# Performance work log

Measured on AMD Instinct MI355X. Metric: run time of the kernel, lower is better.

Reference implementation:

```python
import jax, jax.numpy as jnp
import numpy as np

K = 20  # kNN neighbours (conf.k)

def knn_edge_feats(x, k):
    """x: [B, C, N] -> edge features [B, 2C, N, k] (central || neighbor-central)."""
    xt = jnp.swapaxes(x, 1, 2)                       # [B, N, C]
    sq = jnp.sum(xt * xt, axis=2, keepdims=True)     # [B, N, 1]
    dist = -2.0 * jnp.einsum('bnc,bcm->bnm', xt, x) + sq + jnp.swapaxes(sq, 1, 2)  # [B,N,N]
    idx = jnp.argsort(dist, axis=2)[:, :, 1:k + 1]   # [B, N, k], skip self (col 0)
    nbrs = jax.vmap(lambda xb, ib: xb[:, ib])(x, idx)  # [B, C, N, k]
    central = x[:, :, :, None]                        # [B, C, N, 1]
    return jnp.concatenate([jnp.broadcast_to(central, nbrs.shape), nbrs - central], axis=1)

def edge_conv(x, w, b, k):
    """1x1 conv over edge features, max over k.  x:[B,C,N], w:[Fout,2C], b:[Fout]."""
    ee = knn_edge_feats(x, k)                                   # [B, 2C, N, k]
    y = jnp.einsum('oc,bcnk->bonk', w, ee) + b[None, :, None, None]
    return jnp.max(y, axis=3)                                   # [B, Fout, N]

def setup_inputs() -> dict:
    key = jax.random.key(0)
    ks = iter(jax.random.split(key, 32))
    B, N = 16, 2048
    d = {}
    d['x'] = jax.random.normal(next(ks), (B, 3, N), dtype=jnp.float32)
    def w(shape, scale):
        return jax.random.normal(next(ks), shape, dtype=jnp.float32) * scale
    d['ec0_w'] = w((64, 6), 0.3);    d['ec0_b'] = w((64,), 0.05)
    d['ec1_w'] = w((64, 128), 0.08); d['ec1_b'] = w((64,), 0.05)
    d['ec2_w'] = w((64, 128), 0.08); d['ec2_b'] = w((64,), 0.05)
    d['ec3_w'] = w((128, 128), 0.08); d['ec3_b'] = w((128,), 0.05)
    d['conv0_w'] = w((1024, 320), 0.05); d['conv0_b'] = w((1024,), 0.05)
    d['conv0_s'] = jax.random.uniform(next(ks), (1024,), minval=0.5, maxval=1.5)
    d['conv0_t'] = w((1024,), 0.05)
    d['fc0_w'] = w((512, 1024), 0.03); d['fc0_b'] = w((512,), 0.05)
    d['fc0_s'] = jax.random.uniform(next(ks), (512,), minval=0.5, maxval=1.5)
    d['fc0_t'] = w((512,), 0.05)
    d['fc1_w'] = w((256, 512), 0.04); d['fc1_b'] = w((256,), 0.05)
    d['fc1_s'] = jax.random.uniform(next(ks), (256,), minval=0.5, maxval=1.5)
    d['fc1_t'] = w((256,), 0.05)
    d['fc2_w'] = w((40, 256), 0.06); d['fc2_b'] = w((40,), 0.05)
    d['fc2_s'] = jax.random.uniform(next(ks), (40,), minval=0.5, maxval=1.5)
    d['fc2_t'] = w((40,), 0.05)
    return d

def reference(x, ec0_w, ec0_b, ec1_w, ec1_b, ec2_w, ec2_b, ec3_w, ec3_b,
              conv0_w, conv0_b, conv0_s, conv0_t,
              fc0_w, fc0_b, fc0_s, fc0_t,
              fc1_w, fc1_b, fc1_s, fc1_t,
              fc2_w, fc2_b, fc2_s, fc2_t):
    x1 = edge_conv(x, ec0_w, ec0_b, K)    # [B, 64, N]
    x2 = edge_conv(x1, ec1_w, ec1_b, K)   # [B, 64, N]
    x3 = edge_conv(x2, ec2_w, ec2_b, K)   # [B, 64, N]
    x4 = edge_conv(x3, ec3_w, ec3_b, K)   # [B, 128, N]
    h = jnp.concatenate([x1, x2, x3, x4], axis=1)              # [B, 320, N]
    # conv1dbr: 1x1 conv + BN(affine folded into s,t) + ReLU
    h = jnp.einsum('oc,bcn->bon', conv0_w, h) + conv0_b[None, :, None]
    h = jax.nn.relu(h * conv0_s[None, :, None] + conv0_t[None, :, None])  # [B, 1024, N]
    g = jnp.max(h, axis=2)                                     # [B, 1024]
    # fcbr blocks: linear + BN + ReLU
    g = jax.nn.relu((g @ fc0_w.T + fc0_b) * fc0_s + fc0_t)     # [B, 512]
    g = jax.nn.relu((g @ fc1_w.T + fc1_b) * fc1_s + fc1_t)     # [B, 256]
    g = jax.nn.relu((g @ fc2_w.T + fc2_b) * fc2_s + fc2_t)     # [B, 40]
    return g
```

## Files before the change

### kernel.cpp

```cpp
#include <hip/hip_runtime.h>

#define DEVINL __device__ __forceinline__

static const int NPTS = 2048;

typedef __attribute__((ext_vector_type(8))) short bf16x8;
typedef __attribute__((ext_vector_type(4))) float f32x4;

DEVINL unsigned fenc(float x) {
    int b = __float_as_int(x);
    return (b < 0) ? ~(unsigned)b : ((unsigned)b | 0x80000000u);
}
DEVINL float fdec(unsigned u) {
    return (u & 0x80000000u) ? __int_as_float((int)(u & 0x7fffffffu))
                             : __int_as_float((int)~u);
}
DEVINL unsigned long long u64min(unsigned long long a, unsigned long long b) {
    return (b < a) ? b : a;
}
DEVINL unsigned short f2bf(float x) {
    unsigned u = __float_as_uint(x);
    return (unsigned short)((u + 0x7fffu + ((u >> 16) & 1u)) >> 16);
}
DEVINL float bf2f(unsigned short h) { return __uint_as_float(((unsigned)h) << 16); }

DEVINL void topk20(float v[32], unsigned long long* cand, int lane,
                   int* __restrict__ Iout, int outBase) {
    float t16[16];
#pragma unroll
    for (int i = 0; i < 16; ++i) t16[i] = fminf(v[i], v[i + 16]);
#pragma unroll
    for (int i = 0; i < 8; ++i) t16[i] = fminf(t16[i], t16[i + 8]);
#pragma unroll
    for (int i = 0; i < 4; ++i) t16[i] = fminf(t16[i], t16[i + 4]);
    float s = fminf(fminf(t16[0], t16[1]), fminf(t16[2], t16[3]));
#pragma unroll
    for (int k = 2; k <= 64; k <<= 1) {
#pragma unroll
        for (int j = k >> 1; j >= 1; j >>= 1) {
            float o = __shfl_xor(s, j);
            bool keepmin = (((lane & j) == 0) == ((lane & k) == 0));
            s = keepmin ? fminf(s, o) : fmaxf(s, o);
        }
    }
    const float tau = __shfl(s, 19);
    int cnt = 0;
#pragma unroll
    for (int j = 0; j < 32; ++j) {
        bool pass = (v[j] <= tau);
        unsigned long long mask = __ballot(pass);
        if (pass) {
            int pos = cnt + (int)__popcll(mask & ((1ull << lane) - 1ull));
            if (pos < 64) {
                int col = lane * 4 + (j & 3) + ((j >> 2) << 8);
                cand[pos] = ((unsigned long long)fenc(v[j]) << 32) | (unsigned)col;
            }
        }
        cnt += (int)__popcll(mask);
    }
    if (cnt <= 64) {
        unsigned long long key = (lane < cnt) ? cand[lane] : ~0ull;
#pragma unroll
        for (int k = 2; k <= 64; k <<= 1) {
#pragma unroll
            for (int j = k >> 1; j >= 1; j >>= 1) {
                unsigned long long o = __shfl_xor(key, j);
                bool keepmin = (((lane & j) == 0) == ((lane & k) == 0));
                unsigned long long mn = u64min(key, o);
                unsigned long long mx = (key ^ o) ^ mn;
                key = keepmin ? mn : mx;
            }
        }
        if (lane < 20) Iout[outBase + lane] = (int)(unsigned)(key & 0xffffffffu);
    } else {
        unsigned long long vk[32];
#pragma unroll
        for (int j = 0; j < 32; ++j) {
            int col = lane * 4 + (j & 3) + ((j >> 2) << 8);
            vk[j] = ((unsigned long long)fenc(v[j]) << 32) | (unsigned)col;
        }
        unsigned long long last = 0ull;
        for (int it = 0; it < 20; ++it) {
            unsigned long long q16[16];
#pragma unroll
            for (int i = 0; i < 16; ++i) {
                unsigned long long a = (vk[i] > last) ? vk[i] : ~0ull;
                unsigned long long c = (vk[i + 16] > last) ? vk[i + 16] : ~0ull;
                q16[i] = u64min(a, c);
            }
#pragma unroll
            for (int i = 0; i < 8; ++i) q16[i] = u64min(q16[i], q16[i + 8]);
#pragma unroll
            for (int i = 0; i < 4; ++i) q16[i] = u64min(q16[i], q16[i + 4]);
            unsigned long long best = u64min(u64min(q16[0], q16[1]), u64min(q16[2], q16[3]));
#pragma unroll
            for (int off = 32; off >= 1; off >>= 1) {
                unsigned long long o = __shfl_down(best, off);
                best = u64min(best, o);
            }
            best = __shfl(best, 0);
            if (lane == 0) Iout[outBase + it] = (int)(unsigned)(best & 0xffffffffu);
            last = best;
        }
    }
}

__global__ __launch_bounds__(256) void knnfused_kernel(const float* __restrict__ X, int bs,
                                                       int* __restrict__ Iout) {
    extern __shared__ char smem[];
    float* Dr = (float*)smem;
    float* As = (float*)(smem + 65536);
    unsigned long long* cand = (unsigned long long*)(smem + 67584);
    const int N = NPTS, K = 20;
    const int b = blockIdx.y, n0 = blockIdx.x * 8;
    const float* __restrict__ Xb = X + (size_t)b * bs;
    const int tid = threadIdx.x;
    if (tid < 128) {
        int c = tid >> 1, r4 = (tid & 1) * 4;
        *(float4*)&As[c * 8 + r4] = *(const float4*)&Xb[(size_t)c * N + n0 + r4];
    }
    __syncthreads();
    const int m0 = tid * 4, m1 = 1024 + tid * 4;
    float acc0[8][4], acc1[8][4], sq0[4], sq1[4];
#pragma unroll
    for (int r = 0; r < 8; ++r)
#pragma unroll
        for (int j = 0; j < 4; ++j) { acc0[r][j] = 0.f; acc1[r][j] = 0.f; }
#pragma unroll
    for (int j = 0; j < 4; ++j) { sq0[j] = 0.f; sq1[j] = 0.f; }
#pragma unroll 4
    for (int c = 0; c < 64; ++c) {
        float4 b0 = *(const float4*)&Xb[(size_t)c * N + m0];
        float4 b1 = *(const float4*)&Xb[(size_t)c * N + m1];
        float4 a0 = *(const float4*)&As[c * 8];
        float4 a1 = *(const float4*)&As[c * 8 + 4];
        sq0[0] += b0.x * b0.x; sq0[1] += b0.y * b0.y;
        sq0[2] += b0.z * b0.z; sq0[3] += b0.w * b0.w;
        sq1[0] += b1.x * b1.x; sq1[1] += b1.y * b1.y;
        sq1[2] += b1.z * b1.z; sq1[3] += b1.w * b1.w;
        float av[8] = {a0.x, a0.y, a0.z, a0.w, a1.x, a1.y, a1.z, a1.w};
#pragma unroll
        for (int r = 0; r < 8; ++r) {
            acc0[r][0] += av[r] * b0.x; acc0[r][1] += av[r] * b0.y;
            acc0[r][2] += av[r] * b0.z; acc0[r][3] += av[r] * b0.w;
            acc1[r][0] += av[r] * b1.x; acc1[r][1] += av[r] * b1.y;
            acc1[r][2] += av[r] * b1.z; acc1[r][3] += av[r] * b1.w;
        }
    }
    const float INF = __builtin_inff();
#pragma unroll
    for (int r = 0; r < 8; ++r) {
        const int n = n0 + r;
        float d0[4] = {sq0[0] - 2.f * acc0[r][0], sq0[1] - 2.f * acc0[r][1],
                       sq0[2] - 2.f * acc0[r][2], sq0[3] - 2.f * acc0[r][3]};
        float d1[4] = {sq1[0] - 2.f * acc1[r][0], sq1[1] - 2.f * acc1[r][1],
                       sq1[2] - 2.f * acc1[r][2], sq1[3] - 2.f * acc1[r][3]};
#pragma unroll
        for (int j = 0; j < 4; ++j) {
            if (m0 + j == n) d0[j] = INF;
            if (m1 + j == n) d1[j] = INF;
        }
        *(float4*)&Dr[r * N + m0] = make_float4(d0[0], d0[1], d0[2], d0[3]);
        *(float4*)&Dr[r * N + m1] = make_float4(d1[0], d1[1], d1[2], d1[3]);
    }
    __syncthreads();
    const int w = tid >> 6, lane = tid & 63;
#pragma unroll
    for (int rr = 0; rr < 2; ++rr) {
        const int r = w * 2 + rr;
        const float* __restrict__ rp = &Dr[r * N];
        float v[32];
#pragma unroll
        for (int q = 0; q < 8; ++q) {
            float4 x4 = *(const float4*)&rp[lane * 4 + q * 256];
            v[q * 4 + 0] = x4.x; v[q * 4 + 1] = x4.y;
            v[q * 4 + 2] = x4.z; v[q * 4 + 3] = x4.w;
        }
        topk20(v, cand + w * 64, lane, Iout, (b * N + n0 + r) * K);
    }
}

__global__ __launch_bounds__(256) void select0_kernel(const float* __restrict__ X,
                                                      int* __restrict__ Iout) {
    const int N = NPTS, K = 20;
    __shared__ unsigned long long cand[4][64];
    const int w = threadIdx.x >> 6, lane = threadIdx.x & 63;
    const int rowg = blockIdx.x * 4 + w;
    const int b = rowg >> 11, n = rowg & 2047;
    const float* __restrict__ Xb = X + (size_t)b * 3 * N;
    const float xr = Xb[n], yr = Xb[N + n], zr = Xb[2 * N + n];
    const float INF = __builtin_inff();
    float v[32];
#pragma unroll
    for (int q = 0; q < 8; ++q) {
        const int base = lane * 4 + q * 256;
        const float4 xm = *(const float4*)&Xb[base];
        const float4 ym = *(const float4*)&Xb[N + base];
        const float4 zm = *(const float4*)&Xb[2 * N + base];
        float mx[4] = {xm.x, xm.y, xm.z, xm.w};
        float my[4] = {ym.x, ym.y, ym.z, ym.w};
        float mz[4] = {zm.x, zm.y, zm.z, zm.w};
#pragma unroll
        for (int j = 0; j < 4; ++j) {
            float sq = mx[j] * mx[j] + my[j] * my[j] + mz[j] * mz[j];
            float dot = xr * mx[j] + yr * my[j] + zr * mz[j];
            float d = sq - 2.f * dot;
            v[q * 4 + j] = (base + j == n) ? INF : d;
        }
    }
    topk20(v, &cand[w][0], lane, Iout, (b * N + n) * K);
}

template<int F, int C>
__global__ __launch_bounds__(256) void ut_kernel(const float* __restrict__ X, int bs,
                                                 const float* __restrict__ W,
                                                 const float* __restrict__ bias,
                                                 float* __restrict__ U, float* __restrict__ T) {
    const int N = NPTS;
    __shared__ float Ws2[64][C + 1];
    __shared__ float Wsd[64][C + 1];
    const int n0 = blockIdx.x * 64, f0 = blockIdx.y * 64, b = blockIdx.z;
    const int tid = threadIdx.x;
    for (int i = tid; i < 64 * C; i += 256) {
        int ff = i / C, c = i - ff * C;
        float w1 = W[(f0 + ff) * (2 * C) + c];
        float w2 = W[(f0 + ff) * (2 * C) + C + c];
        Ws2[ff][c] = w2;
        Wsd[ff][c] = w1 - w2;
    }
    __syncthreads();
    const int nt = tid & 15, fg = tid >> 4;
    const float* __restrict__ Xb = X + (size_t)b * bs;
    float au[4][4], av[4][4];
#pragma unroll
    for (int i = 0; i < 4; ++i)
#pragma unroll
        for (int j = 0; j < 4; ++j) { au[i][j] = 0.f; av[i][j] = 0.f; }
#pragma unroll 4
    for (int c = 0; c < C; ++c) {
        const float4 xv = *(const float4*)&Xb[(size_t)c * N + n0 + nt * 4];
#pragma unroll
        for (int fi = 0; fi < 4; ++fi) {
            float w2v = Ws2[fg * 4 + fi][c];
            float wdv = Wsd[fg * 4 + fi][c];
            au[fi][0] += w2v * xv.x; au[fi][1] += w2v * xv.y;
            au[fi][2] += w2v * xv.z; au[fi][3] += w2v * xv.w;
            av[fi][0] += wdv * xv.x; av[fi][1] += wdv * xv.y;
            av[fi][2] += wdv * xv.z; av[fi][3] += wdv * xv.w;
        }
    }
#pragma unroll
    for (int ni = 0; ni < 4; ++ni) {
        int n = n0 + nt * 4 + ni;
        float4 uv = make_float4(au[0][ni], au[1][ni], au[2][ni], au[3][ni]);
        *(float4*)&U[((size_t)b * N + n) * F + f0 + fg * 4] = uv;
    }
#pragma unroll
    for (int fi = 0; fi < 4; ++fi) {
        int f = f0 + fg * 4 + fi;
        float bv = bias[f];
        float4 tv = make_float4(av[fi][0] + bv, av[fi][1] + bv, av[fi][2] + bv, av[fi][3] + bv);
        *(float4*)&T[((size_t)b * F + f) * N + n0 + nt * 4] = tv;
    }
}

template<int F, bool WRITE_F32>
__global__ __launch_bounds__(256) void gathermax_kernel(const float* __restrict__ U,
                                                        const float* __restrict__ T,
                                                        const int* __restrict__ idx,
                                                        float* __restrict__ Y, int bsY,
                                                        unsigned short* __restrict__ HtH,
                                                        unsigned short* __restrict__ HtL,
                                                        int hoff) {
    const int N = NPTS, K = 20, FG = F / 8;
    __shared__ int sidx[32 * 20];
    const int b = blockIdx.y, n0 = blockIdx.x * 32, tid = threadIdx.x;
    const int p = tid >> 3, fg = tid & 7;
    for (int t = tid; t < 32 * K; t += 256) sidx[t] = idx[(b * N + n0) * K + t];
    __syncthreads();
    const int n = n0 + p;
    const float* __restrict__ Ub = U + (size_t)b * N * F;
    const int fbase = fg * FG;
    float mx[FG];
#pragma unroll
    for (int i = 0; i < FG; ++i) mx[i] = -__builtin_inff();
#pragma unroll 4
    for (int j = 0; j < K; ++j) {
        const int r = sidx[p * K + j];
        const float4* up = (const float4*)&Ub[(size_t)r * F + fbase];
#pragma unroll
        for (int q = 0; q < FG / 4; ++q) {
            float4 a = up[q];
            mx[q * 4 + 0] = fmaxf(mx[q * 4 + 0], a.x);
            mx[q * 4 + 1] = fmaxf(mx[q * 4 + 1], a.y);
            mx[q * 4 + 2] = fmaxf(mx[q * 4 + 2], a.z);
            mx[q * 4 + 3] = fmaxf(mx[q * 4 + 3], a.w);
        }
    }
    float val[FG];
#pragma unroll
    for (int i = 0; i < FG; ++i) {
        const int f = fbase + i;
        val[i] = T[((size_t)b * F + f) * N + n] + mx[i];
        if (WRITE_F32) Y[(size_t)b * bsY + (size_t)f * N + n] = val[i];
    }
    unsigned short hs[FG], ls[FG];
#pragma unroll
    for (int i = 0; i < FG; ++i) {
        unsigned short h = f2bf(val[i]);
        hs[i] = h;
        ls[i] = f2bf(val[i] - bf2f(h));
    }
    const size_t hb = ((size_t)b * N + n) * 320 + hoff + fbase;
#pragma unroll
    for (int q = 0; q < FG / 8; ++q) {
        *(int4*)&HtH[hb + q * 8] = *(const int4*)&hs[q * 8];
        *(int4*)&HtL[hb + q * 8] = *(const int4*)&ls[q * 8];
    }
}

__global__ __launch_bounds__(256) void wsplit_kernel(const float* __restrict__ W,
                                                     unsigned short* __restrict__ WH,
                                                     unsigned short* __restrict__ WL) {
    const int e = blockIdx.x * 256 + threadIdx.x;
    float w = W[e];
    unsigned short h = f2bf(w);
    WH[e] = h;
    WL[e] = f2bf(w - bf2f(h));
}

__global__ __launch_bounds__(256) void conv0mfma_kernel(const unsigned short* __restrict__ HtH,
                                                        const unsigned short* __restrict__ HtL,
                                                        const unsigned short* __restrict__ WH,
                                                        const unsigned short* __restrict__ WL,
                                                        unsigned* __restrict__ M) {
    const int N = NPTS;
    __shared__ unsigned short HsH[64][40], HsL[64][40], WsH[128][40], WsL[128][40];
    const int n0 = blockIdx.x * 64, f0 = blockIdx.y * 128, b = blockIdx.z;
    const int tid = threadIdx.x;
    const int wave = tid >> 6, lane = tid & 63;
    const int wm = wave & 1, wf = wave >> 1;
    const int row = lane & 15, quad = lane >> 4;
    f32x4 acc[2][4];
#pragma unroll
    for (int i = 0; i < 2; ++i)
#pragma unroll
        for (int j = 0; j < 4; ++j) acc[i][j] = (f32x4){0.f, 0.f, 0.f, 0.f};

    const int hn = tid >> 2, hq = tid & 3;
    const int wfr = tid >> 1, wq = tid & 1;

    for (int c0 = 0; c0 < 320; c0 += 32) {
        {
            const size_t src = ((size_t)b * N + n0 + hn) * 320 + c0 + hq * 8;
            *(int4*)&HsH[hn][hq * 8] = *(const int4*)&HtH[src];
            *(int4*)&HsL[hn][hq * 8] = *(const int4*)&HtL[src];
        }
        {
            const size_t src = (size_t)(f0 + wfr) * 320 + c0 + wq * 16;
            *(int4*)&WsH[wfr][wq * 16]     = *(const int4*)&WH[src];
            *(int4*)&WsH[wfr][wq * 16 + 8] = *(const int4*)&WH[src + 8];
            *(int4*)&WsL[wfr][wq * 16]     = *(const int4*)&WL[src];
            *(int4*)&WsL[wfr][wq * 16 + 8] = *(const int4*)&WL[src + 8];
        }
        __syncthreads();
        bf16x8 aH[2], aL[2];
#pragma unroll
        for (int mt = 0; mt < 2; ++mt) {
            aH[mt] = *(const bf16x8*)&HsH[wm * 32 + mt * 16 + row][quad * 8];
            aL[mt] = *(const bf16x8*)&HsL[wm * 32 + mt * 16 + row][quad * 8];
        }
#pragma unroll
        for (int nt = 0; nt < 4; ++nt) {
            bf16x8 bH = *(const bf16x8*)&WsH[wf * 64 + nt * 16 + row][quad * 8];
            bf16x8 bL = *(const bf16x8*)&WsL[wf * 64 + nt * 16 + row][quad * 8];
#pragma unroll
            for (int mt = 0; mt < 2; ++mt) {
                acc[mt][nt] = __builtin_amdgcn_mfma_f32_16x16x32_bf16(aH[mt], bH, acc[mt][nt], 0, 0, 0);
                acc[mt][nt] = __builtin_amdgcn_mfma_f32_16x16x32_bf16(aH[mt], bL, acc[mt][nt], 0, 0, 0);
                acc[mt][nt] = __builtin_amdgcn_mfma_f32_16x16x32_bf16(aL[mt], bH, acc[mt][nt], 0, 0, 0);
            }
        }
        __syncthreads();
    }
#pragma unroll
    for (int nt = 0; nt < 4; ++nt) {
        float m = acc[0][nt][0];
#pragma unroll
        for (int r = 1; r < 4; ++r) m = fmaxf(m, acc[0][nt][r]);
#pragma unroll
        for (int r = 0; r < 4; ++r) m = fmaxf(m, acc[1][nt][r]);
        m = fmaxf(m, __shfl_down(m, 16));
        m = fmaxf(m, __shfl_down(m, 32));
        if (quad == 0)
            atomicMax(&M[(b << 10) + f0 + wf * 64 + nt * 16 + row], fenc(m));
    }
}

__global__ __launch_bounds__(256) void fc_kernel(const unsigned* __restrict__ M,
    const float* __restrict__ cb, const float* __restrict__ cs, const float* __restrict__ ct,
    const float* __restrict__ w0, const float* __restrict__ b0, const float* __restrict__ s0, const float* __restrict__ t0,
    const float* __restrict__ w1, const float* __restrict__ b1, const float* __restrict__ s1, const float* __restrict__ t1,
    const float* __restrict__ w2, const float* __restrict__ b2, const float* __restrict__ s2, const float* __restrict__ t2,
    float* __restrict__ out) {
    __shared__ float g0[1024], g1[512], g2[256];
    const int b = blockIdx.x, tid = threadIdx.x;
    for (int f = tid; f < 1024; f += 256) {
        float z = fdec(M[b * 1024 + f]);
        float g = cs[f] * (z + cb[f]) + ct[f];
        g0[f] = fmaxf(g, 0.f);
    }
    __syncthreads();
    for (int f = tid; f < 512; f += 256) {
        const float4* wp = (const float4*)(w0 + (size_t)f * 1024);
        float acc = 0.f;
#pragma unroll 4
        for (int c = 0; c < 256; ++c) {
            float4 wv = wp[c];
            float4 gv = *(const float4*)&g0[c * 4];
            acc += wv.x * gv.x + wv.y * gv.y + wv.z * gv.z + wv.w * gv.w;
        }
        float g = s0[f] * (acc + b0[f]) + t0[f];
        g1[f] = fmaxf(g, 0.f);
    }
    __syncthreads();
    if (tid < 256) {
        const float4* wp = (const float4*)(w1 + (size_t)tid * 512);
        float acc = 0.f;
#pragma unroll 4
        for (int c = 0; c < 128; ++c) {
            float4 wv = wp[c];
            float4 gv = *(const float4*)&g1[c * 4];
            acc += wv.x * gv.x + wv.y * gv.y + wv.z * gv.z + wv.w * gv.w;
        }
        float g = s1[tid] * (acc + b1[tid]) + t1[tid];
        g2[tid] = fmaxf(g, 0.f);
    }
    __syncthreads();
    if (tid < 40) {
        const float4* wp = (const float4*)(w2 + (size_t)tid * 256);
        float acc = 0.f;
#pragma unroll 4
        for (int c = 0; c < 64; ++c) {
            float4 wv = wp[c];
            float4 gv = *(const float4*)&g2[c * 4];
            acc += wv.x * gv.x + wv.y * gv.y + wv.z * gv.z + wv.w * gv.w;
        }
        float g = s2[tid] * (acc + b2[tid]) + t2[tid];
        out[b * 40 + tid] = fmaxf(g, 0.f);
    }
}

extern "C" void kernel_launch(void* const* d_in, const int* in_sizes, int n_in,
                              void* d_out, int out_size, void* d_ws, size_t ws_size,
                              hipStream_t stream) {
    const float* x       = (const float*)d_in[0];
    const float* ec0_w   = (const float*)d_in[1];
    const float* ec0_b   = (const float*)d_in[2];
    const float* ec1_w   = (const float*)d_in[3];
    const float* ec1_b   = (const float*)d_in[4];
    const float* ec2_w   = (const float*)d_in[5];
    const float* ec2_b   = (const float*)d_in[6];
    const float* ec3_w   = (const float*)d_in[7];
    const float* ec3_b   = (const float*)d_in[8];
    const float* conv0_w = (const float*)d_in[9];
    const float* conv0_b = (const float*)d_in[10];
    const float* conv0_s = (const float*)d_in[11];
    const float* conv0_t = (const float*)d_in[12];
    const float* fc0_w   = (const float*)d_in[13];
    const float* fc0_b   = (const float*)d_in[14];
    const float* fc0_s   = (const float*)d_in[15];
    const float* fc0_t   = (const float*)d_in[16];
    const float* fc1_w   = (const float*)d_in[17];
    const float* fc1_b   = (const float*)d_in[18];
    const float* fc1_s   = (const float*)d_in[19];
    const float* fc1_t   = (const float*)d_in[20];
    const float* fc2_w   = (const float*)d_in[21];
    const float* fc2_b   = (const float*)d_in[22];
    const float* fc2_s   = (const float*)d_in[23];
    const float* fc2_t   = (const float*)d_in[24];
    float* out = (float*)d_out;

    char* ws = (char*)d_ws;
    const int B = 16, N = NPTS;
    float* Hc   = (float*)(ws + 0);
    float* U    = (float*)(ws + 41943040);
    float* T    = (float*)(ws + 58720256);
    int*   I    = (int*)  (ws + 75497472);
    unsigned* M = (unsigned*)(ws + 78118912);
    unsigned short* W_hi = (unsigned short*)(ws + 78184448);
    unsigned short* W_lo = (unsigned short*)(ws + 78839808);
    unsigned short* HtH  = (unsigned short*)(ws + 79495168);
    unsigned short* HtL  = (unsigned short*)(ws + 100466688);

    (void)hipFuncSetAttribute((const void*)knnfused_kernel,
                              hipFuncAttributeMaxDynamicSharedMemorySize, 69632);

    dim3 blk(256);
    const int bsX0 = 3 * N, bsH = 320 * N;

    wsplit_kernel<<<dim3(1024 * 320 / 256), blk, 0, stream>>>(conv0_w, W_hi, W_lo);

    select0_kernel<<<dim3(B * N / 4), blk, 0, stream>>>(x, I);
    ut_kernel<64, 3><<<dim3(N / 64, 1, B), blk, 0, stream>>>(x, bsX0, ec0_w, ec0_b, U, T);
    gathermax_kernel<64, true><<<dim3(N / 32, B), blk, 0, stream>>>(U, T, I, Hc, bsH, HtH, HtL, 0);

    const float* Xin[3] = {Hc, Hc + (size_t)64 * N, Hc + (size_t)128 * N};
    const float* ecw[3] = {ec1_w, ec2_w, ec3_w};
    const float* ecb[3] = {ec1_b, ec2_b, ec3_b};
    for (int L = 0; L < 3; ++L) {
        knnfused_kernel<<<dim3(N / 8, B), blk, 69632, stream>>>(Xin[L], bsH, I);
        if (L < 2) {
            ut_kernel<64, 64><<<dim3(N / 64, 1, B), blk, 0, stream>>>(Xin[L], bsH, ecw[L], ecb[L], U, T);
            gathermax_kernel<64, true><<<dim3(N / 32, B), blk, 0, stream>>>(
                U, T, I, Hc + (size_t)(64 * (L + 1)) * N, bsH, HtH, HtL, 64 * (L + 1));
        } else {
            ut_kernel<128, 64><<<dim3(N / 64, 2, B), blk, 0, stream>>>(Xin[L], bsH, ecw[L], ecb[L], U, T);
            gathermax_kernel<128, false><<<dim3(N / 32, B), blk, 0, stream>>>(
                U, T, I, Hc + (size_t)192 * N, bsH, HtH, HtL, 192);
        }
    }

    (void)hipMemsetAsync(M, 0, B * 1024 * sizeof(unsigned), stream);
    conv0mfma_kernel<<<dim3(N / 64, 1024 / 128, B), blk, 0, stream>>>(HtH, HtL, W_hi, W_lo, M);

    fc_kernel<<<dim3(B), blk, 0, stream>>>(M, conv0_b, conv0_s, conv0_t,
                                           fc0_w, fc0_b, fc0_s, fc0_t,
                                           fc1_w, fc1_b, fc1_s, fc1_t,
                                           fc2_w, fc2_b, fc2_s, fc2_t, out);
}
```

Measured before the change: 995.4 us.

## Split kNN distance tile into two halves with per-half top-20 and merge

The fused kNN kernel now computes the 8x2048 distance tile in two passes of 1024 columns, halving shared memory for the tile and the accumulator registers. Each half gets its own top-20 selection: a bitonic sort of per-lane minima sets a threshold, then ballot compaction and a 64-wide bitonic sort, with an iterative fallback when too many candidates pass. The two partial top-20 lists are then merged with a bitonic sort across the wave. The aim is higher occupancy from lower LDS and register use, at the cost of extra sort work, an extra barrier per pass, and the B-operand global loads now issued across two serial passes instead of interleaved in one.

Result: slower. 1.076 ms (+8.1%).

```diff
diff --git a/kernel.cpp b/kernel.cpp
--- a/kernel.cpp
+++ b/kernel.cpp
@@ -105,12 +105,91 @@
     }
 }
 
+DEVINL unsigned long long topk20half(float v[16], int colBase,
+                                     unsigned long long* cand, int lane) {
+    float t8[8];
+#pragma unroll
+    for (int i = 0; i < 8; ++i) t8[i] = fminf(v[i], v[i + 8]);
+#pragma unroll
+    for (int i = 0; i < 4; ++i) t8[i] = fminf(t8[i], t8[i + 4]);
+    float s = fminf(fminf(t8[0], t8[1]), fminf(t8[2], t8[3]));
+#pragma unroll
+    for (int k = 2; k <= 64; k <<= 1) {
+#pragma unroll
+        for (int j = k >> 1; j >= 1; j >>= 1) {
+            float o = __shfl_xor(s, j);
+            bool keepmin = (((lane & j) == 0) == ((lane & k) == 0));
+            s = keepmin ? fminf(s, o) : fmaxf(s, o);
+        }
+    }
+    const float tau = __shfl(s, 19);
+    int cnt = 0;
+#pragma unroll
+    for (int j = 0; j < 16; ++j) {
+        bool pass = (v[j] <= tau);
+        unsigned long long mask = __ballot(pass);
+        if (pass) {
+            int pos = cnt + (int)__popcll(mask & ((1ull << lane) - 1ull));
+            if (pos < 64) {
+                int col = colBase + lane * 4 + (j & 3) + ((j >> 2) << 8);
+                cand[pos] = ((unsigned long long)fenc(v[j]) << 32) | (unsigned)col;
+            }
+        }
+        cnt += (int)__popcll(mask);
+    }
+    if (cnt <= 64) {
+        unsigned long long key = (lane < cnt) ? cand[lane] : ~0ull;
+#pragma unroll
+        for (int k = 2; k <= 64; k <<= 1) {
+#pragma unroll
+            for (int j = k >> 1; j >= 1; j >>= 1) {
+                unsigned long long o = __shfl_xor(key, j);
+                bool keepmin = (((lane & j) == 0) == ((lane & k) == 0));
+                unsigned long long mn = u64min(key, o);
+                unsigned long long mx = (key ^ o) ^ mn;
+                key = keepmin ? mn : mx;
+            }
+        }
+        if (lane >= 20) key = ~0ull;
+        return key;
+    } else {
+        unsigned long long vk[16];
+#pragma unroll
+        for (int j = 0; j < 16; ++j) {
+            int col = colBase + lane * 4 + (j & 3) + ((j >> 2) << 8);
+            vk[j] = ((unsigned long long)fenc(v[j]) << 32) | (unsigned)col;
+        }
+        unsigned long long mykey = ~0ull, last = 0ull;
+        for (int it = 0; it < 20; ++it) {
+            unsigned long long q8[8];
+#pragma unroll
+            for (int i = 0; i < 8; ++i) {
+                unsigned long long a = (vk[i] > last) ? vk[i] : ~0ull;
+                unsigned long long c = (vk[i + 8] > last) ? vk[i + 8] : ~0ull;
+                q8[i] = u64min(a, c);
+            }
+#pragma unroll
+            for (int i = 0; i < 4; ++i) q8[i] = u64min(q8[i], q8[i + 4]);
+            unsigned long long best = u64min(u64min(q8[0], q8[1]), u64min(q8[2], q8[3]));
+#pragma unroll
+            for (int off = 32; off >= 1; off >>= 1) {
+                unsigned long long o = __shfl_down(best, off);
+                best = u64min(best, o);
+            }
+            best = __shfl(best, 0);
+            if (lane == it) mykey = best;
+            last = best;
+        }
+        return mykey;
+    }
+}
+
 __global__ __launch_bounds__(256) void knnfused_kernel(const float* __restrict__ X, int bs,
                                                        int* __restrict__ Iout) {
     extern __shared__ char smem[];
     float* Dr = (float*)smem;
-    float* As = (float*)(smem + 65536);
-    unsigned long long* cand = (unsigned long long*)(smem + 67584);
+    float* As = (float*)(smem + 32768);
+    unsigned long long* cand = (unsigned long long*)(smem + 34816);
     const int N = NPTS, K = 20;
     const int b = blockIdx.y, n0 = blockIdx.x * 8;
     const float* __restrict__ Xb = X + (size_t)b * bs;
@@ -120,63 +199,79 @@
         *(float4*)&As[c * 8 + r4] = *(const float4*)&Xb[(size_t)c * N + n0 + r4];
     }
     __syncthreads();
-    const int m0 = tid * 4, m1 = 1024 + tid * 4;
-    float acc0[8][4], acc1[8][4], sq0[4], sq1[4];
-#pragma unroll
-    for (int r = 0; r < 8; ++r)
-#pragma unroll
-        for (int j = 0; j < 4; ++j) { acc0[r][j] = 0.f; acc1[r][j] = 0.f; }
-#pragma unroll
-    for (int j = 0; j < 4; ++j) { sq0[j] = 0.f; sq1[j] = 0.f; }
+    const int w = tid >> 6, lane = tid & 63;
+    unsigned long long keyA[2], keyB[2];
+
+#pragma unroll 1
+    for (int pass = 0; pass < 2; ++pass) {
+        const int mg = pass * 1024 + tid * 4;
+        float acc[8][4], sq[4];
+#pragma unroll
+        for (int r = 0; r < 8; ++r)
+#pragma unroll
+            for (int j = 0; j < 4; ++j) acc[r][j] = 0.f;
+#pragma unroll
+        for (int j = 0; j < 4; ++j) sq[j] = 0.f;
 #pragma unroll 4
-    for (int c = 0; c < 64; ++c) {
-        float4 b0 = *(const float4*)&Xb[(size_t)c * N + m0];
-        float4 b1 = *(const float4*)&Xb[(size_t)c * N + m1];
-        float4 a0 = *(const float4*)&As[c * 8];
-        float4 a1 = *(const float4*)&As[c * 8 + 4];
-        sq0[0] += b0.x * b0.x; sq0[1] += b0.y * b0.y;
-        sq0[2] += b0.z * b0.z; sq0[3] += b0.w * b0.w;
-        sq1[0] += b1.x * b1.x; sq1[1] += b1.y * b1.y;
-        sq1[2] += b1.z * b1.z; sq1[3] += b1.w * b1.w;
-        float av[8] = {a0.x, a0.y, a0.z, a0.w, a1.x, a1.y, a1.z, a1.w};
+        for (int c = 0; c < 64; ++c) {
+            float4 bv = *(const float4*)&Xb[(size_t)c * N + mg];
+            float4 a0 = *(const float4*)&As[c * 8];
+            float4 a1 = *(const float4*)&As[c * 8 + 4];
+            sq[0] += bv.x * bv.x; sq[1] += bv.y * bv.y;
+            sq[2] += bv.z * bv.z; sq[3] += bv.w * bv.w;
+            float av[8] = {a0.x, a0.y, a0.z, a0.w, a1.x, a1.y, a1.z, a1.w};
+#pragma unroll
+            for (int r = 0; r < 8; ++r) {
+                acc[r][0] += av[r] * bv.x; acc[r][1] += av[r] * bv.y;
+                acc[r][2] += av[r] * bv.z; acc[r][3] += av[r] * bv.w;
+            }
+        }
+        const float INF = __builtin_inff();
 #pragma unroll
         for (int r = 0; r < 8; ++r) {
-            acc0[r][0] += av[r] * b0.x; acc0[r][1] += av[r] * b0.y;
-            acc0[r][2] += av[r] * b0.z; acc0[r][3] += av[r] * b0.w;
-            acc1[r][0] += av[r] * b1.x; acc1[r][1] += av[r] * b1.y;
-            acc1[r][2] += av[r] * b1.z; acc1[r][3] += av[r] * b1.w;
-        }
-    }
-    const float INF = __builtin_inff();
-#pragma unroll
-    for (int r = 0; r < 8; ++r) {
-        const int n = n0 + r;
-        float d0[4] = {sq0[0] - 2.f * acc0[r][0], sq0[1] - 2.f * acc0[r][1],
-                       sq0[2] - 2.f * acc0[r][2], sq0[3] - 2.f * acc0[r][3]};
-        float d1[4] = {sq1[0] - 2.f * acc1[r][0], sq1[1] - 2.f * acc1[r][1],
-                       sq1[2] - 2.f * acc1[r][2], sq1[3] - 2.f * acc1[r][3]};
-#pragma unroll
-        for (int j = 0; j < 4; ++j) {
-            if (m0 + j == n) d0[j] = INF;
-            if (m1 + j == n) d1[j] = INF;
-        }
-        *(float4*)&Dr[r * N + m0] = make_float4(d0[0], d0[1], d0[2], d0[3]);
-        *(float4*)&Dr[r * N + m1] = make_float4(d1[0], d1[1], d1[2], d1[3]);
-    }
-    __syncthreads();
-    const int w = tid >> 6, lane = tid & 63;
+            const int n = n0 + r;
+            float d[4] = {sq[0] - 2.f * acc[r][0], sq[1] - 2.f * acc[r][1],
+                          sq[2] - 2.f * acc[r][2], sq[3] - 2.f * acc[r][3]};
+#pragma unroll
+            for (int j = 0; j < 4; ++j)
+                if (mg + j == n) d[j] = INF;
+            *(float4*)&Dr[r * 1024 + tid * 4] = make_float4(d[0], d[1], d[2], d[3]);
+        }
+        __syncthreads();
+#pragma unroll
+        for (int rr = 0; rr < 2; ++rr) {
+            const int r = w * 2 + rr;
+            const float* __restrict__ rp = &Dr[r * 1024];
+            float v[16];
+#pragma unroll
+            for (int q = 0; q < 4; ++q) {
+                float4 x4 = *(const float4*)&rp[lane * 4 + q * 256];
+                v[q * 4 + 0] = x4.x; v[q * 4 + 1] = x4.y;
+                v[q * 4 + 2] = x4.z; v[q * 4 + 3] = x4.w;
+            }
+            unsigned long long kk = topk20half(v, pass * 1024, cand + w * 64, lane);
+            if (pass == 0) keyA[rr] = kk; else keyB[rr] = kk;
+        }
+        __syncthreads();
+    }
 #pragma unroll
     for (int rr = 0; rr < 2; ++rr) {
-        const int r = w * 2 + rr;
-        const float* __restrict__ rp = &Dr[r * N];
-        float v[32];
-#pragma unroll
-        for (int q = 0; q < 8; ++q) {
-            float4 x4 = *(const float4*)&rp[lane * 4 + q * 256];
-            v[q * 4 + 0] = x4.x; v[q * 4 + 1] = x4.y;
-            v[q * 4 + 2] = x4.z; v[q * 4 + 3] = x4.w;
-        }
-        topk20(v, cand + w * 64, lane, Iout, (b * N + n0 + r) * K);
+        unsigned long long kb = __shfl(keyB[rr], lane - 32);
+        unsigned long long key = (lane < 20) ? keyA[rr]
+                               : (lane >= 32 && lane < 52) ? kb : ~0ull;
+#pragma unroll
+        for (int k = 2; k <= 64; k <<= 1) {
+#pragma unroll
+            for (int j = k >> 1; j >= 1; j >>= 1) {
+                unsigned long long o = __shfl_xor(key, j);
+                bool keepmin = (((lane & j) == 0) == ((lane & k) == 0));
+                unsigned long long mn = u64min(key, o);
+                unsigned long long mx = (key ^ o) ^ mn;
+                key = keepmin ? mn : mx;
+            }
+        }
+        if (lane < 20)
+            Iout[(b * N + n0 + w * 2 + rr) * K + lane] = (int)(unsigned)(key & 0xffffffffu);
     }
 }
 
@@ -494,7 +589,7 @@
     unsigned short* HtL  = (unsigned short*)(ws + 100466688);
 
     (void)hipFuncSetAttribute((const void*)knnfused_kernel,
-                              hipFuncAttributeMaxDynamicSharedMemorySize, 69632);
+                              hipFuncAttributeMaxDynamicSharedMemorySize, 36864);
 
     dim3 blk(256);
     const int bsX0 = 3 * N, bsH = 320 * N;
@@ -509,7 +604,7 @@
     const float* ecw[3] = {ec1_w, ec2_w, ec3_w};
     const float* ecb[3] = {ec1_b, ec2_b, ec3_b};
     for (int L = 0; L < 3; ++L) {
-        knnfused_kernel<<<dim3(N / 8, B), blk, 69632, stream>>>(Xin[L], bsH, I);
+        knnfused_kernel<<<dim3(N / 8, B), blk, 36864, stream>>>(Xin[L], bsH, I);
         if (L < 2) {
             ut_kernel<64, 64><<<dim3(N / 64, 1, B), blk, 0, stream>>>(Xin[L], bsH, ecw[L], ecb[L], U, T);
             gathermax_kernel<64, true><<<dim3(N / 32, B), blk, 0, stream>>>(
```

## Compute kNN distances with split-bf16 MFMA, then refine candidates in exact fp32

Applied to the files above, without the earlier changes.

Replaces the scalar-FMA distance kernel for layers 1-3 with an MFMA kernel that builds dot products from the hi/lo bf16 split copies of the features. A bitonic sort finds the approximate 21st-smallest distance, and every point within an error margin of it is kept as a candidate. Distances for those candidates are recomputed in fp32 and sorted to pick the exact top-20. A new per-point squared-norm and max-norm kernel feeds the margin. This trades most of the fp32 ALU work for matrix-core work, at the risk of dropping true neighbours if more than 64 candidates pass the cutoff or the margin is too tight.

After: 1.221 ms. 1.23x slower.

```diff
diff --git a/kernel.cpp b/kernel.cpp
--- a/kernel.cpp
+++ b/kernel.cpp
@@ -105,78 +105,149 @@
     }
 }
 
-__global__ __launch_bounds__(256) void knnfused_kernel(const float* __restrict__ X, int bs,
-                                                       int* __restrict__ Iout) {
+__global__ __launch_bounds__(256) void sqmax_kernel(const float* __restrict__ X, int bs,
+                                                    float* __restrict__ sqOut,
+                                                    unsigned* __restrict__ Rsq) {
+    const int N = NPTS;
+    const int b = blockIdx.y, m = blockIdx.x * 256 + threadIdx.x;
+    const float* __restrict__ Xb = X + (size_t)b * bs;
+    float s = 0.f;
+#pragma unroll 8
+    for (int c = 0; c < 64; ++c) { float t = Xb[(size_t)c * N + m]; s = fmaf(t, t, s); }
+    sqOut[(b << 11) + m] = s;
+    float mx = s;
+#pragma unroll
+    for (int off = 32; off >= 1; off >>= 1) mx = fmaxf(mx, __shfl_down(mx, off));
+    if ((threadIdx.x & 63) == 0) atomicMax(&Rsq[b], __float_as_uint(mx));
+}
+
+__global__ __launch_bounds__(512) void knnmfma_kernel(
+    const unsigned short* __restrict__ HtH, const unsigned short* __restrict__ HtL,
+    int hoff, const float* __restrict__ Xf, int bsX,
+    const float* __restrict__ sqB, const unsigned* __restrict__ Rsq,
+    int* __restrict__ Iout) {
     extern __shared__ char smem[];
     float* Dr = (float*)smem;
-    float* As = (float*)(smem + 65536);
-    unsigned long long* cand = (unsigned long long*)(smem + 67584);
-    const int N = NPTS, K = 20;
-    const int b = blockIdx.y, n0 = blockIdx.x * 8;
-    const float* __restrict__ Xb = X + (size_t)b * bs;
-    const int tid = threadIdx.x;
-    if (tid < 128) {
-        int c = tid >> 1, r4 = (tid & 1) * 4;
-        *(float4*)&As[c * 8 + r4] = *(const float4*)&Xb[(size_t)c * N + n0 + r4];
-    }
-    __syncthreads();
-    const int m0 = tid * 4, m1 = 1024 + tid * 4;
-    float acc0[8][4], acc1[8][4], sq0[4], sq1[4];
-#pragma unroll
-    for (int r = 0; r < 8; ++r)
-#pragma unroll
-        for (int j = 0; j < 4; ++j) { acc0[r][j] = 0.f; acc1[r][j] = 0.f; }
-#pragma unroll
-    for (int j = 0; j < 4; ++j) { sq0[j] = 0.f; sq1[j] = 0.f; }
-#pragma unroll 4
-    for (int c = 0; c < 64; ++c) {
-        float4 b0 = *(const float4*)&Xb[(size_t)c * N + m0];
-        float4 b1 = *(const float4*)&Xb[(size_t)c * N + m1];
-        float4 a0 = *(const float4*)&As[c * 8];
-        float4 a1 = *(const float4*)&As[c * 8 + 4];
-        sq0[0] += b0.x * b0.x; sq0[1] += b0.y * b0.y;
-        sq0[2] += b0.z * b0.z; sq0[3] += b0.w * b0.w;
-        sq1[0] += b1.x * b1.x; sq1[1] += b1.y * b1.y;
-        sq1[2] += b1.z * b1.z; sq1[3] += b1.w * b1.w;
-        float av[8] = {a0.x, a0.y, a0.z, a0.w, a1.x, a1.y, a1.z, a1.w};
-#pragma unroll
-        for (int r = 0; r < 8; ++r) {
-            acc0[r][0] += av[r] * b0.x; acc0[r][1] += av[r] * b0.y;
-            acc0[r][2] += av[r] * b0.z; acc0[r][3] += av[r] * b0.w;
-            acc1[r][0] += av[r] * b1.x; acc1[r][1] += av[r] * b1.y;
-            acc1[r][2] += av[r] * b1.z; acc1[r][3] += av[r] * b1.w;
-        }
-    }
-    const float INF = __builtin_inff();
-#pragma unroll
-    for (int r = 0; r < 8; ++r) {
-        const int n = n0 + r;
-        float d0[4] = {sq0[0] - 2.f * acc0[r][0], sq0[1] - 2.f * acc0[r][1],
-                       sq0[2] - 2.f * acc0[r][2], sq0[3] - 2.f * acc0[r][3]};
-        float d1[4] = {sq1[0] - 2.f * acc1[r][0], sq1[1] - 2.f * acc1[r][1],
-                       sq1[2] - 2.f * acc1[r][2], sq1[3] - 2.f * acc1[r][3]};
-#pragma unroll
-        for (int j = 0; j < 4; ++j) {
-            if (m0 + j == n) d0[j] = INF;
-            if (m1 + j == n) d1[j] = INF;
-        }
-        *(float4*)&Dr[r * N + m0] = make_float4(d0[0], d0[1], d0[2], d0[3]);
-        *(float4*)&Dr[r * N + m1] = make_float4(d1[0], d1[1], d1[2], d1[3]);
-    }
-    __syncthreads();
-    const int w = tid >> 6, lane = tid & 63;
+    int* cand = (int*)(smem + 65792);
+    const int N = NPTS, K = 20, DS = 1028;
+    const int b = blockIdx.y, n0 = blockIdx.x * 16;
+    const int tid = threadIdx.x, wave = tid >> 6, lane = tid & 63;
+    const int fr = lane & 15, quad = lane >> 4;
+    const float Rmax = sqrtf(__uint_as_float(Rsq[b]));
+
+    const size_t abase = ((size_t)(b * N + n0 + fr)) * 320 + hoff + quad * 8;
+    const bf16x8 aH0 = *(const bf16x8*)&HtH[abase];
+    const bf16x8 aH1 = *(const bf16x8*)&HtH[abase + 32];
+    const bf16x8 aL0 = *(const bf16x8*)&HtL[abase];
+    const bf16x8 aL1 = *(const bf16x8*)&HtL[abase + 32];
+
+    float v[2][2][16];
+#pragma unroll
+    for (int pass = 0; pass < 2; ++pass) {
+#pragma unroll 2
+        for (int tt = 0; tt < 8; ++tt) {
+            const int m0 = pass * 1024 + wave * 128 + tt * 16;
+            const size_t bbase = ((size_t)(b * N + m0 + fr)) * 320 + hoff + quad * 8;
+            bf16x8 bH0 = *(const bf16x8*)&HtH[bbase];
+            bf16x8 bH1 = *(const bf16x8*)&HtH[bbase + 32];
+            bf16x8 bL0 = *(const bf16x8*)&HtL[bbase];
+            bf16x8 bL1 = *(const bf16x8*)&HtL[bbase + 32];
+            f32x4 acc = (f32x4){0.f, 0.f, 0.f, 0.f};
+            acc = __builtin_amdgcn_mfma_f32_16x16x32_bf16(aH0, bH0, acc, 0, 0, 0);
+            acc = __builtin_amdgcn_mfma_f32_16x16x32_bf16(aH1, bH1, acc, 0, 0, 0);
+            acc = __builtin_amdgcn_mfma_f32_16x16x32_bf16(aH0, bL0, acc, 0, 0, 0);
+            acc = __builtin_amdgcn_mfma_f32_16x16x32_bf16(aH1, bL1, acc, 0, 0, 0);
+            acc = __builtin_amdgcn_mfma_f32_16x16x32_bf16(aL0, bH0, acc, 0, 0, 0);
+            acc = __builtin_amdgcn_mfma_f32_16x16x32_bf16(aL1, bH1, acc, 0, 0, 0);
+            const float sqv = sqB[(b << 11) + m0 + fr];
+            const int mloc = wave * 128 + tt * 16 + fr;
+#pragma unroll
+            for (int r = 0; r < 4; ++r)
+                Dr[(quad * 4 + r) * DS + mloc] = sqv - 2.f * acc[r];
+        }
+        __syncthreads();
+#pragma unroll
+        for (int rr = 0; rr < 2; ++rr) {
+            const float* __restrict__ rp = &Dr[(wave * 2 + rr) * DS];
+#pragma unroll
+            for (int q = 0; q < 4; ++q) {
+                float4 x4 = *(const float4*)&rp[lane * 4 + q * 256];
+                v[pass][rr][q * 4 + 0] = x4.x; v[pass][rr][q * 4 + 1] = x4.y;
+                v[pass][rr][q * 4 + 2] = x4.z; v[pass][rr][q * 4 + 3] = x4.w;
+            }
+        }
+        __syncthreads();
+    }
+
+    int cntk[2];
 #pragma unroll
     for (int rr = 0; rr < 2; ++rr) {
-        const int r = w * 2 + rr;
-        const float* __restrict__ rp = &Dr[r * N];
-        float v[32];
-#pragma unroll
-        for (int q = 0; q < 8; ++q) {
-            float4 x4 = *(const float4*)&rp[lane * 4 + q * 256];
-            v[q * 4 + 0] = x4.x; v[q * 4 + 1] = x4.y;
-            v[q * 4 + 2] = x4.z; v[q * 4 + 3] = x4.w;
-        }
-        topk20(v, cand + w * 64, lane, Iout, (b * N + n0 + r) * K);
+        const int nrow = n0 + wave * 2 + rr;
+        float lm = v[0][rr][0];
+#pragma unroll
+        for (int j = 1; j < 16; ++j) lm = fminf(lm, v[0][rr][j]);
+#pragma unroll
+        for (int j = 0; j < 16; ++j) lm = fminf(lm, v[1][rr][j]);
+        float s = lm;
+#pragma unroll
+        for (int k = 2; k <= 64; k <<= 1) {
+#pragma unroll
+            for (int j = k >> 1; j >= 1; j >>= 1) {
+                float o = __shfl_xor(s, j);
+                bool keepmin = (((lane & j) == 0) == ((lane & k) == 0));
+                s = keepmin ? fminf(s, o) : fmaxf(s, o);
+            }
+        }
+        const float tau21 = __shfl(s, 20);
+        const float sqn = sqB[(b << 11) + nrow];
+        const float margin = 3e-4f * sqrtf(fmaxf(sqn, 0.f)) * Rmax + 1e-12f;
+        const float cutoff = tau21 + 2.f * margin;
+        int cnt = 0;
+        int* cl = &cand[(wave * 2 + rr) * 64];
+#pragma unroll
+        for (int pass = 0; pass < 2; ++pass) {
+#pragma unroll
+            for (int j = 0; j < 16; ++j) {
+                bool p = (v[pass][rr][j] <= cutoff);
+                unsigned long long mask = __ballot(p);
+                if (p) {
+                    int pos = cnt + (int)__popcll(mask & ((1ull << lane) - 1ull));
+                    if (pos < 64)
+                        cl[pos] = pass * 1024 + lane * 4 + (j & 3) + ((j >> 2) << 8);
+                }
+                cnt += (int)__popcll(mask);
+            }
+        }
+        cntk[rr] = (cnt > 64) ? 64 : cnt;
+    }
+
+    const float* __restrict__ Xb = Xf + (size_t)b * bsX;
+#pragma unroll 1
+    for (int rr = 0; rr < 2; ++rr) {
+        const int nrow = n0 + wave * 2 + rr;
+        const int cnt = cntk[rr];
+        unsigned long long key = ~0ull;
+        if (lane < cnt) {
+            const int m = cand[(wave * 2 + rr) * 64 + lane];
+            float acc = 0.f;
+#pragma unroll 8
+            for (int c = 0; c < 64; ++c)
+                acc = fmaf(Xb[(size_t)c * N + nrow], Xb[(size_t)c * N + m], acc);
+            const float d = sqB[(b << 11) + m] - 2.f * acc;
+            key = ((unsigned long long)fenc(d) << 32) | (unsigned)m;
+        }
+#pragma unroll
+        for (int k = 2; k <= 64; k <<= 1) {
+#pragma unroll
+            for (int j = k >> 1; j >= 1; j >>= 1) {
+                unsigned long long o = __shfl_xor(key, j);
+                bool keepmin = (((lane & j) == 0) == ((lane & k) == 0));
+                unsigned long long mn = u64min(key, o);
+                key = keepmin ? mn : ((key ^ o) ^ mn);
+            }
+        }
+        if (lane >= 1 && lane < 21)
+            Iout[(b * N + nrow) * K + (lane - 1)] = (int)(unsigned)(key & 0xffffffffu);
     }
 }
 
@@ -492,9 +563,11 @@
     unsigned short* W_lo = (unsigned short*)(ws + 78839808);
     unsigned short* HtH  = (unsigned short*)(ws + 79495168);
     unsigned short* HtL  = (unsigned short*)(ws + 100466688);
-
-    (void)hipFuncSetAttribute((const void*)knnfused_kernel,
-                              hipFuncAttributeMaxDynamicSharedMemorySize, 69632);
+    float* sqb  = (float*)(ws + 121438208);
+    unsigned* Rsq = (unsigned*)(ws + 121569280);
+
+    (void)hipFuncSetAttribute((const void*)knnmfma_kernel,
+                              hipFuncAttributeMaxDynamicSharedMemorySize, 69888);
 
     dim3 blk(256);
     const int bsX0 = 3 * N, bsH = 320 * N;
@@ -509,7 +582,10 @@
     const float* ecw[3] = {ec1_w, ec2_w, ec3_w};
     const float* ecb[3] = {ec1_b, ec2_b, ec3_b};
     for (int L = 0; L < 3; ++L) {
-        knnfused_kernel<<<dim3(N / 8, B), blk, 69632, stream>>>(Xin[L], bsH, I);
+        (void)hipMemsetAsync(Rsq, 0, B * sizeof(unsigned), stream);
+        sqmax_kernel<<<dim3(N / 256, B), blk, 0, stream>>>(Xin[L], bsH, sqb, Rsq);
+        knnmfma_kernel<<<dim3(N / 16, B), dim3(512), 69888, stream>>>(
+            HtH, HtL, 64 * L, Xin[L], bsH, sqb, Rsq, I);
         if (L < 2) {
             ut_kernel<64, 64><<<dim3(N / 64, 1, B), blk, 0, stream>>>(Xin[L], bsH, ecw[L], ecb[L], U, T);
             gathermax_kernel<64, true><<<dim3(N / 32, B), blk, 0, stream>>>(
```
